# Kernel optimization log

Hardware: AMD Instinct MI355X
Metric: run time of the kernel (lower is better)

The kernel has to match this reference:

```python
import jax, jax.numpy as jnp
import numpy as np

IN_DIM = 768
D_MODEL = 256
B, T = 64, 2048
LN_EPS = 1e-5


def setup_inputs() -> dict:
    key = jax.random.key(0)
    ks = jax.random.split(key, 8)
    s_in = 1.0 / np.sqrt(IN_DIM)
    s_d = 1.0 / np.sqrt(D_MODEL)
    return {
        "x": jax.random.normal(ks[0], (B, T, IN_DIM), dtype=jnp.float32),
        "ln_gamma": jnp.ones((IN_DIM,), jnp.float32),
        "ln_beta": jnp.zeros((IN_DIM,), jnp.float32),
        "W_proj": jax.random.uniform(ks[1], (IN_DIM, D_MODEL), jnp.float32, -s_in, s_in),
        "b_proj": jax.random.uniform(ks[2], (D_MODEL,), jnp.float32, -s_in, s_in),
        "W1": jax.random.uniform(ks[3], (D_MODEL, D_MODEL), jnp.float32, -s_d, s_d),
        "b1": jax.random.uniform(ks[4], (D_MODEL,), jnp.float32, -s_d, s_d),
        "W2": jax.random.uniform(ks[5], (D_MODEL,), jnp.float32, -s_d, s_d),
        "b2": jax.random.uniform(ks[6], (), jnp.float32, -s_d, s_d),
    }


def reference(x, ln_gamma, ln_beta, W_proj, b_proj, W1, b1, W2, b2):
    # nan/inf sanitization to 0
    x = jnp.nan_to_num(x, nan=0.0, posinf=0.0, neginf=0.0)
    # LayerNorm over last dim (biased variance, eps=1e-5)
    mu = jnp.mean(x, axis=-1, keepdims=True)
    var = jnp.mean(jnp.square(x - mu), axis=-1, keepdims=True)
    xn = (x - mu) * jax.lax.rsqrt(var + LN_EPS) * ln_gamma + ln_beta
    # projection to d_model: [B, T, D]
    h = jnp.einsum('btf,fd->btd', xn, W_proj) + b_proj
    # tanh-MLP attention scores: [B, T]
    a = jnp.tanh(jnp.einsum('btd,de->bte', h, W1) + b1)
    w = jnp.einsum('bte,e->bt', a, W2) + b2
    w = jax.nn.softmax(w, axis=-1)
    # weighted-sum pooling over T: [B, D]
    return jnp.einsum('btd,bt->bd', h, w)
```

## Files before the change

### kernel.cpp

```cpp
#include <hip/hip_runtime.h>

#define LN_EPS 1e-5f

typedef __attribute__((ext_vector_type(8))) short s8vec;
typedef __attribute__((ext_vector_type(4))) float f4vec;

#define OFF_WPT   0u
#define OFF_W1T   393216u
#define OFF_U     524288u
#define OFF_C     525312u
#define OFF_UPART 526336u
#define OFF_VPART 575488u
#define OFF_PM    624640u
#define OFF_PS    632832u
#define OFF_PO    641024u

#define BAR()     asm volatile("s_barrier" ::: "memory")
#define WAIT_V4() asm volatile("s_waitcnt vmcnt(4) lgkmcnt(0)" ::: "memory")
#define WAIT_V0() asm volatile("s_waitcnt vmcnt(0) lgkmcnt(0)" ::: "memory")
#define WAIT_L0() asm volatile("s_waitcnt lgkmcnt(0)" ::: "memory")
#define ORDER_FENCE() do { asm volatile("" ::: "memory"); \
                           __builtin_amdgcn_sched_barrier(0); } while (0)

__device__ __forceinline__ unsigned short f2bf(float f) {
  unsigned int u = __float_as_uint(f);
  u += 0x7fffu + ((u >> 16) & 1u);
  return (unsigned short)(u >> 16);
}
__device__ __forceinline__ float bf2f(unsigned short h) {
  return __uint_as_float(((unsigned int)h) << 16);
}
__device__ __forceinline__ void gll16(const void* g, void* l) {
  __builtin_amdgcn_global_load_lds(
      (const __attribute__((address_space(1))) unsigned int*)g,
      (__attribute__((address_space(3))) unsigned int*)l, 16, 0, 0);
}

__global__ void k0_prep(const float* __restrict__ Wp,
                        const float* __restrict__ gamma,
                        const float* __restrict__ beta,
                        const float* __restrict__ W1,
                        char* __restrict__ ws) {
  const int blk = blockIdx.x;
  const int n = threadIdx.x;
  const int sw = (n & 7) << 4;
  if (blk < 48) {
    unsigned short* wpt = (unsigned short*)(ws + OFF_WPT);
    const int k0 = blk * 16;
    float up = 0.f, vp = 0.f;
#pragma unroll
    for (int j = 0; j < 16; ++j) {
      const int k = k0 + j;
      const float w = Wp[k * 256 + n];
      const float wpv = gamma[k] * w;
      up += wpv;
      vp += beta[k] * w;
      const int c = k >> 6, kc = k & 63;
      wpt[c * 16384 + n * 64 + ((((kc * 2) ^ sw)) >> 1)] = f2bf(wpv);
    }
    ((float*)(ws + OFF_UPART))[blk * 256 + n] = up;
    ((float*)(ws + OFF_VPART))[blk * 256 + n] = vp;
  } else {
    unsigned short* w1t = (unsigned short*)(ws + OFF_W1T);
    const int d0 = (blk - 48) * 16;
#pragma unroll
    for (int j = 0; j < 16; ++j) {
      const int d = d0 + j;
      const int c = d >> 6, dc = d & 63;
      w1t[c * 16384 + n * 64 + ((((dc * 2) ^ sw)) >> 1)] = f2bf(W1[d * 256 + n]);
    }
  }
}

__global__ void k0_reduce(const float* __restrict__ bproj, char* __restrict__ ws) {
  const int n = threadIdx.x;
  const float* upart = (const float*)(ws + OFF_UPART);
  const float* vpart = (const float*)(ws + OFF_VPART);
  float u = 0.f, v = 0.f;
  for (int i = 0; i < 48; ++i) {
    u += upart[i * 256 + n];
    v += vpart[i * 256 + n];
  }
  ((float*)(ws + OFF_U))[n] = u;
  ((float*)(ws + OFF_C))[n] = v + bproj[n];
}

__global__ __launch_bounds__(256, 2)
void k1_main(const float* __restrict__ x,
             const float* __restrict__ b1,
             const float* __restrict__ W2,
             char* __restrict__ ws) {
  __shared__ __align__(16) char sm_h[32768];
  __shared__ __align__(16) char sm_b[32768];
  __shared__ __align__(16) char sm_a[8192];
  __shared__ float sm_u[256], sm_c[256], sm_b1[256], sm_w2[256];
  __shared__ float sm_mu[64], sm_inv[64];
  __shared__ float sm_lp[64 * 4];
  __shared__ float sm_lg[64];
  __shared__ float sm_e[64];

  const int tid  = threadIdx.x;
  const int lane = tid & 63;
  const int wid  = tid >> 6;
  const int lr = lane & 15;
  const int lq = lane >> 4;

  sm_u[tid]  = ((const float*)(ws + OFF_U))[tid];
  sm_c[tid]  = ((const float*)(ws + OFF_C))[tid];
  sm_b1[tid] = b1[tid];
  sm_w2[tid] = W2[tid];

  const int arow = tid >> 2;
  const int aq   = tid & 3;
  const float* xrow = x + (size_t)(blockIdx.x * 64 + arow) * 768 + aq * 16;

  const char* bsrc  = (const char*)ws + OFF_WPT + wid * 8192 + lane * 16;
  const char* b2src = (const char*)ws + OFF_W1T + wid * 8192 + lane * 16;
  char*       bdst  = sm_b + wid * 8192 + lane * 16;

  const f4vec fz = {0.f, 0.f, 0.f, 0.f};
  f4vec acc[4][4];
#pragma unroll
  for (int m = 0; m < 4; ++m)
#pragma unroll
    for (int n = 0; n < 4; ++n) acc[m][n] = fz;

  float s1 = 0.f, s2 = 0.f;
  float4 vaA[4], vaB[4];
#pragma unroll
  for (int j = 0; j < 4; ++j) vaA[j] = *(const float4*)(xrow + 0 * 64 + j * 4);
#pragma unroll
  for (int j = 0; j < 4; ++j) vaB[j] = *(const float4*)(xrow + 1 * 64 + j * 4);

  auto p1body = [&](int c, float4 (&va)[4], bool pf) {
#pragma unroll
    for (int s = 0; s < 8; ++s) gll16(bsrc + c * 32768 + s * 1024, bdst + s * 1024);
    ORDER_FENCE();
    float v[16];
#pragma unroll
    for (int j = 0; j < 4; ++j) {
      v[4*j+0] = va[j].x; v[4*j+1] = va[j].y; v[4*j+2] = va[j].z; v[4*j+3] = va[j].w;
    }
    unsigned int pk[8];
#pragma unroll
    for (int j = 0; j < 16; ++j) {
      float f = v[j];
      if ((__float_as_uint(f) & 0x7f800000u) == 0x7f800000u) f = 0.f;
      s1 += f; s2 += f * f;
      const unsigned int hb = f2bf(f);
      if ((j & 1) == 0) pk[j >> 1] = hb; else pk[j >> 1] |= hb << 16;
    }
    {
      const int base = arow * 128 + aq * 32;
      const int sw = (arow & 7) << 4;
      *(int4*)(sm_a + ((base     ) ^ sw)) = make_int4((int)pk[0], (int)pk[1], (int)pk[2], (int)pk[3]);
      *(int4*)(sm_a + ((base + 16) ^ sw)) = make_int4((int)pk[4], (int)pk[5], (int)pk[6], (int)pk[7]);
    }
    if (pf) {
#pragma unroll
      for (int j = 0; j < 4; ++j) va[j] = *(const float4*)(xrow + (c + 2) * 64 + j * 4);
    }
    if (pf) WAIT_V4(); else WAIT_V0();
    BAR();
#pragma unroll
    for (int ks = 0; ks < 2; ++ks) {
      const int kb = (ks * 32 + lq * 8) * 2;
      s8vec af[4], bfv[4];
#pragma unroll
      for (int m = 0; m < 4; ++m) {
        const int row = m * 16 + lr;
        af[m] = *(const s8vec*)(sm_a + ((row * 128 + kb) ^ ((row & 7) << 4)));
      }
#pragma unroll
      for (int n = 0; n < 4; ++n) {
        const int row = wid * 64 + n * 16 + lr;
        bfv[n] = *(const s8vec*)(sm_b + ((row * 128 + kb) ^ ((row & 7) << 4)));
      }
#pragma unroll
      for (int m = 0; m < 4; ++m)
#pragma unroll
        for (int n = 0; n < 4; ++n)
          acc[m][n] = __builtin_amdgcn_mfma_f32_16x16x32_bf16(af[m], bfv[n], acc[m][n], 0, 0, 0);
    }
    BAR();
  };

  for (int cc = 0; cc < 12; cc += 2) {
    p1body(cc,     vaA, cc + 2 < 12);
    p1body(cc + 1, vaB, cc + 3 < 12);
  }

  s1 += __shfl_xor(s1, 1); s1 += __shfl_xor(s1, 2);
  s2 += __shfl_xor(s2, 1); s2 += __shfl_xor(s2, 2);
  if (aq == 0) {
    const float mu = s1 * (1.f / 768.f);
    float var = s2 * (1.f / 768.f) - mu * mu;
    var = fmaxf(var, 0.f);
    sm_mu[arow]  = mu;
    sm_inv[arow] = rsqrtf(var + LN_EPS);
  }
#pragma unroll
  for (int s = 0; s < 8; ++s) gll16(b2src + s * 1024, bdst + s * 1024);
  WAIT_L0();
  BAR();

#pragma unroll
  for (int m = 0; m < 4; ++m) {
#pragma unroll
    for (int i = 0; i < 4; ++i) {
      const int rl = m * 16 + lq * 4 + i;
      const float mu  = sm_mu[rl];
      const float inv = sm_inv[rl];
      const int sw = (rl & 7) << 4;
#pragma unroll
      for (int n = 0; n < 4; ++n) {
        const int cd = wid * 64 + n * 16 + lr;
        const float h = inv * (acc[m][n][i] - mu * sm_u[cd]) + sm_c[cd];
        *(unsigned short*)(sm_h + ((rl * 512 + cd * 2) ^ sw)) = f2bf(h);
      }
    }
  }
  WAIT_V0();
  BAR();

  f4vec acc2[4][4];
#pragma unroll
  for (int m = 0; m < 4; ++m)
#pragma unroll
    for (int n = 0; n < 4; ++n) acc2[m][n] = fz;

  for (int c = 0; c < 4; ++c) {
    s8vec af[2][4], bfv[2][4];
#pragma unroll
    for (int ks = 0; ks < 2; ++ks) {
      const int kh = (c * 64 + ks * 32 + lq * 8) * 2;
      const int kb = (ks * 32 + lq * 8) * 2;
#pragma unroll
      for (int m = 0; m < 4; ++m) {
        const int row = m * 16 + lr;
        af[ks][m] = *(const s8vec*)(sm_h + ((row * 512 + kh) ^ ((row & 7) << 4)));
      }
#pragma unroll
      for (int n = 0; n < 4; ++n) {
        const int row = wid * 64 + n * 16 + lr;
        bfv[ks][n] = *(const s8vec*)(sm_b + ((row * 128 + kb) ^ ((row & 7) << 4)));
      }
    }
    WAIT_L0();
    BAR();
    if (c < 3) {
#pragma unroll
      for (int s = 0; s < 8; ++s) gll16(b2src + (c + 1) * 32768 + s * 1024, bdst + s * 1024);
    }
#pragma unroll
    for (int ks = 0; ks < 2; ++ks)
#pragma unroll
      for (int m = 0; m < 4; ++m)
#pragma unroll
        for (int n = 0; n < 4; ++n)
          acc2[m][n] = __builtin_amdgcn_mfma_f32_16x16x32_bf16(af[ks][m], bfv[ks][n], acc2[m][n], 0, 0, 0);
    if (c < 3) WAIT_V0();
    BAR();
  }

  float lp[4][4];
#pragma unroll
  for (int m = 0; m < 4; ++m)
#pragma unroll
    for (int i = 0; i < 4; ++i) lp[m][i] = 0.f;

#pragma unroll
  for (int m = 0; m < 4; ++m) {
#pragma unroll
    for (int n = 0; n < 4; ++n) {
      const int cd = wid * 64 + n * 16 + lr;
      const float b1v = sm_b1[cd];
      const float w2v = sm_w2[cd];
#pragma unroll
      for (int i = 0; i < 4; ++i) {
        float z = acc2[m][n][i] + b1v;
        z = fminf(fmaxf(z, -15.f), 15.f);
        const float e2 = __expf(2.f * z);
        const float a = (e2 - 1.f) / (e2 + 1.f);
        lp[m][i] += a * w2v;
      }
    }
  }
#pragma unroll
  for (int m = 0; m < 4; ++m) {
#pragma unroll
    for (int i = 0; i < 4; ++i) {
      float t = lp[m][i];
      t += __shfl_xor(t, 1);
      t += __shfl_xor(t, 2);
      t += __shfl_xor(t, 4);
      t += __shfl_xor(t, 8);
      if (lr == 0) sm_lp[(m * 16 + lq * 4 + i) * 4 + wid] = t;
    }
  }
  __syncthreads();
  if (tid < 64)
    sm_lg[tid] = sm_lp[tid*4+0] + sm_lp[tid*4+1] + sm_lp[tid*4+2] + sm_lp[tid*4+3];
  __syncthreads();

  float mx = -1e30f;
  for (int r = 0; r < 64; ++r) mx = fmaxf(mx, sm_lg[r]);
  if (tid < 64) sm_e[tid] = __expf(sm_lg[tid] - mx);
  __syncthreads();

  {
    const int d = tid;
    float o = 0.f;
    for (int r = 0; r < 64; ++r) {
      const float ev = sm_e[r];
      const unsigned short hb =
          *(const unsigned short*)(sm_h + ((r * 512 + d * 2) ^ ((r & 7) << 4)));
      o += ev * bf2f(hb);
    }
    ((float*)(ws + OFF_PO))[blockIdx.x * 256 + d] = o;
  }
  if (tid == 0) {
    float s = 0.f;
    for (int r = 0; r < 64; ++r) s += sm_e[r];
    ((float*)(ws + OFF_PS))[blockIdx.x] = s;
    ((float*)(ws + OFF_PM))[blockIdx.x] = mx;
  }
}

__global__ void k2_combine(const char* __restrict__ ws, float* __restrict__ out) {
  const int b = blockIdx.x;
  const int d = threadIdx.x;
  const float* pm = (const float*)(ws + OFF_PM) + b * 32;
  const float* ps = (const float*)(ws + OFF_PS) + b * 32;
  const float* po = (const float*)(ws + OFF_PO) + (size_t)b * 32 * 256;
  float mx = -1e30f;
  for (int c = 0; c < 32; ++c) mx = fmaxf(mx, pm[c]);
  float num = 0.f, den = 0.f;
  for (int c = 0; c < 32; ++c) {
    const float al = __expf(pm[c] - mx);
    den += al * ps[c];
    num += al * po[c * 256 + d];
  }
  out[b * 256 + d] = num / den;
}

extern "C" void kernel_launch(void* const* d_in, const int* in_sizes, int n_in,
                              void* d_out, int out_size, void* d_ws, size_t ws_size,
                              hipStream_t stream) {
  const float* x     = (const float*)d_in[0];
  const float* gamma = (const float*)d_in[1];
  const float* beta  = (const float*)d_in[2];
  const float* Wp    = (const float*)d_in[3];
  const float* bproj = (const float*)d_in[4];
  const float* W1    = (const float*)d_in[5];
  const float* b1    = (const float*)d_in[6];
  const float* W2    = (const float*)d_in[7];
  char* ws = (char*)d_ws;
  float* out = (float*)d_out;

  k0_prep   <<<dim3(64),   dim3(256), 0, stream>>>(Wp, gamma, beta, W1, ws);
  k0_reduce <<<dim3(1),    dim3(256), 0, stream>>>(bproj, ws);
  k1_main   <<<dim3(2048), dim3(256), 0, stream>>>(x, b1, W2, ws);
  k2_combine<<<dim3(64),   dim3(256), 0, stream>>>(ws, out);
}
```

Baseline: 170.4 us.

## Double-buffer LDS for phase-1 GEMM with 32-wide K chunks and MFMA priority

The first GEMM (LayerNorm'd x times W_proj) now works in 32-column K chunks with ping-pong LDS buffers for both A and B. Staging the next chunk's weights and packing the next x chunk now overlap the MFMAs on the current buffer, and each step needs only one barrier instead of two. The prep kernel writes W_proj in a matching 32-column swizzled layout, and s_setprio raises wave priority around the MFMA blocks in both GEMMs. The cost is twice as many loop iterations with smaller per-step work, more barriers overall, and a narrower 4-way XOR swizzle that may bring back LDS bank conflicts.

```diff
diff --git a/kernel.cpp b/kernel.cpp
--- a/kernel.cpp
+++ b/kernel.cpp
@@ -16,7 +16,7 @@
 #define OFF_PO    641024u
 
 #define BAR()     asm volatile("s_barrier" ::: "memory")
-#define WAIT_V4() asm volatile("s_waitcnt vmcnt(4) lgkmcnt(0)" ::: "memory")
+#define WAIT_V2() asm volatile("s_waitcnt vmcnt(2) lgkmcnt(0)" ::: "memory")
 #define WAIT_V0() asm volatile("s_waitcnt vmcnt(0) lgkmcnt(0)" ::: "memory")
 #define WAIT_L0() asm volatile("s_waitcnt lgkmcnt(0)" ::: "memory")
 #define ORDER_FENCE() do { asm volatile("" ::: "memory"); \
@@ -43,9 +43,9 @@
                         char* __restrict__ ws) {
   const int blk = blockIdx.x;
   const int n = threadIdx.x;
-  const int sw = (n & 7) << 4;
   if (blk < 48) {
     unsigned short* wpt = (unsigned short*)(ws + OFF_WPT);
+    const int sw = (n & 3) << 4;
     const int k0 = blk * 16;
     float up = 0.f, vp = 0.f;
 #pragma unroll
@@ -55,13 +55,14 @@
       const float wpv = gamma[k] * w;
       up += wpv;
       vp += beta[k] * w;
-      const int c = k >> 6, kc = k & 63;
-      wpt[c * 16384 + n * 64 + ((((kc * 2) ^ sw)) >> 1)] = f2bf(wpv);
+      const int c = k >> 5, kc = k & 31;
+      wpt[c * 8192 + n * 32 + ((((kc * 2) ^ sw)) >> 1)] = f2bf(wpv);
     }
     ((float*)(ws + OFF_UPART))[blk * 256 + n] = up;
     ((float*)(ws + OFF_VPART))[blk * 256 + n] = vp;
   } else {
     unsigned short* w1t = (unsigned short*)(ws + OFF_W1T);
+    const int sw = (n & 7) << 4;
     const int d0 = (blk - 48) * 16;
 #pragma unroll
     for (int j = 0; j < 16; ++j) {
@@ -112,11 +113,10 @@
 
   const int arow = tid >> 2;
   const int aq   = tid & 3;
-  const float* xrow = x + (size_t)(blockIdx.x * 64 + arow) * 768 + aq * 16;
-
-  const char* bsrc  = (const char*)ws + OFF_WPT + wid * 8192 + lane * 16;
+  const float* xrow = x + (size_t)(blockIdx.x * 64 + arow) * 768 + aq * 8;
+
+  const char* bsrc  = (const char*)ws + OFF_WPT + wid * 4096 + lane * 16;
   const char* b2src = (const char*)ws + OFF_W1T + wid * 8192 + lane * 16;
-  char*       bdst  = sm_b + wid * 8192 + lane * 16;
 
   const f4vec fz = {0.f, 0.f, 0.f, 0.f};
   f4vec acc[4][4];
@@ -126,69 +126,84 @@
     for (int n = 0; n < 4; ++n) acc[m][n] = fz;
 
   float s1 = 0.f, s2 = 0.f;
-  float4 vaA[4], vaB[4];
-#pragma unroll
-  for (int j = 0; j < 4; ++j) vaA[j] = *(const float4*)(xrow + 0 * 64 + j * 4);
-#pragma unroll
-  for (int j = 0; j < 4; ++j) vaB[j] = *(const float4*)(xrow + 1 * 64 + j * 4);
-
-  auto p1body = [&](int c, float4 (&va)[4], bool pf) {
-#pragma unroll
-    for (int s = 0; s < 8; ++s) gll16(bsrc + c * 32768 + s * 1024, bdst + s * 1024);
-    ORDER_FENCE();
-    float v[16];
-#pragma unroll
-    for (int j = 0; j < 4; ++j) {
-      v[4*j+0] = va[j].x; v[4*j+1] = va[j].y; v[4*j+2] = va[j].z; v[4*j+3] = va[j].w;
-    }
-    unsigned int pk[8];
-#pragma unroll
-    for (int j = 0; j < 16; ++j) {
+  float4 xcE[2], xcO[2];
+  xcE[0] = *(const float4*)(xrow + 0);  xcE[1] = *(const float4*)(xrow + 4);
+  xcO[0] = *(const float4*)(xrow + 32); xcO[1] = *(const float4*)(xrow + 36);
+
+  auto stageB = [&](int t, int p) {
+#pragma unroll
+    for (int s = 0; s < 4; ++s)
+      gll16(bsrc + t * 16384 + s * 1024,
+            sm_b + p * 16384 + wid * 4096 + s * 1024 + lane * 16);
+  };
+  auto packA = [&](const float4 (&xc)[2], int p) {
+    float v[8];
+    v[0]=xc[0].x; v[1]=xc[0].y; v[2]=xc[0].z; v[3]=xc[0].w;
+    v[4]=xc[1].x; v[5]=xc[1].y; v[6]=xc[1].z; v[7]=xc[1].w;
+    unsigned int pk[4];
+#pragma unroll
+    for (int j = 0; j < 8; ++j) {
       float f = v[j];
       if ((__float_as_uint(f) & 0x7f800000u) == 0x7f800000u) f = 0.f;
       s1 += f; s2 += f * f;
       const unsigned int hb = f2bf(f);
       if ((j & 1) == 0) pk[j >> 1] = hb; else pk[j >> 1] |= hb << 16;
     }
-    {
-      const int base = arow * 128 + aq * 32;
-      const int sw = (arow & 7) << 4;
-      *(int4*)(sm_a + ((base     ) ^ sw)) = make_int4((int)pk[0], (int)pk[1], (int)pk[2], (int)pk[3]);
-      *(int4*)(sm_a + ((base + 16) ^ sw)) = make_int4((int)pk[4], (int)pk[5], (int)pk[6], (int)pk[7]);
-    }
-    if (pf) {
-#pragma unroll
-      for (int j = 0; j < 4; ++j) va[j] = *(const float4*)(xrow + (c + 2) * 64 + j * 4);
-    }
-    if (pf) WAIT_V4(); else WAIT_V0();
+    *(int4*)(sm_a + p * 4096 + ((arow * 64 + aq * 16) ^ ((arow & 3) << 4))) =
+        make_int4((int)pk[0], (int)pk[1], (int)pk[2], (int)pk[3]);
+  };
+  auto mfmaStep = [&](int p) {
+    s8vec af[4], bf[4];
+#pragma unroll
+    for (int m = 0; m < 4; ++m) {
+      const int row = m * 16 + lr;
+      af[m] = *(const s8vec*)(sm_a + p * 4096 +
+                              ((row * 64 + lq * 16) ^ ((row & 3) << 4)));
+    }
+#pragma unroll
+    for (int n = 0; n < 4; ++n) {
+      const int row = wid * 64 + n * 16 + lr;
+      bf[n] = *(const s8vec*)(sm_b + p * 16384 +
+                              ((row * 64 + lq * 16) ^ ((row & 3) << 4)));
+    }
+    __builtin_amdgcn_s_setprio(1);
+#pragma unroll
+    for (int m = 0; m < 4; ++m)
+#pragma unroll
+      for (int n = 0; n < 4; ++n)
+        acc[m][n] = __builtin_amdgcn_mfma_f32_16x16x32_bf16(af[m], bf[n], acc[m][n], 0, 0, 0);
+    __builtin_amdgcn_s_setprio(0);
+  };
+
+  stageB(0, 0); ORDER_FENCE();
+  packA(xcE, 0);
+  xcE[0] = *(const float4*)(xrow + 64); xcE[1] = *(const float4*)(xrow + 68);
+  WAIT_V2(); BAR();
+
+  for (int t = 0; t < 22; t += 2) {
+    stageB(t + 1, 1); ORDER_FENCE();
+    packA(xcO, 1);
+    xcO[0] = *(const float4*)(xrow + (t + 3) * 32);
+    xcO[1] = *(const float4*)(xrow + (t + 3) * 32 + 4);
+    mfmaStep(0);
+    WAIT_V2(); BAR();
+
+    stageB(t + 2, 0); ORDER_FENCE();
+    packA(xcE, 0);
+    if (t + 4 <= 23) {
+      xcE[0] = *(const float4*)(xrow + (t + 4) * 32);
+      xcE[1] = *(const float4*)(xrow + (t + 4) * 32 + 4);
+    }
+    mfmaStep(1);
+    if (t + 4 <= 23) WAIT_V2(); else WAIT_V0();
     BAR();
-#pragma unroll
-    for (int ks = 0; ks < 2; ++ks) {
-      const int kb = (ks * 32 + lq * 8) * 2;
-      s8vec af[4], bfv[4];
-#pragma unroll
-      for (int m = 0; m < 4; ++m) {
-        const int row = m * 16 + lr;
-        af[m] = *(const s8vec*)(sm_a + ((row * 128 + kb) ^ ((row & 7) << 4)));
-      }
-#pragma unroll
-      for (int n = 0; n < 4; ++n) {
-        const int row = wid * 64 + n * 16 + lr;
-        bfv[n] = *(const s8vec*)(sm_b + ((row * 128 + kb) ^ ((row & 7) << 4)));
-      }
-#pragma unroll
-      for (int m = 0; m < 4; ++m)
-#pragma unroll
-        for (int n = 0; n < 4; ++n)
-          acc[m][n] = __builtin_amdgcn_mfma_f32_16x16x32_bf16(af[m], bfv[n], acc[m][n], 0, 0, 0);
-    }
-    BAR();
-  };
-
-  for (int cc = 0; cc < 12; cc += 2) {
-    p1body(cc,     vaA, cc + 2 < 12);
-    p1body(cc + 1, vaB, cc + 3 < 12);
-  }
+  }
+  stageB(23, 1); ORDER_FENCE();
+  packA(xcO, 1);
+  mfmaStep(0);
+  WAIT_V0(); BAR();
+  mfmaStep(1);
+  BAR();
 
   s1 += __shfl_xor(s1, 1); s1 += __shfl_xor(s1, 2);
   s2 += __shfl_xor(s2, 1); s2 += __shfl_xor(s2, 2);
@@ -200,7 +215,8 @@
     sm_inv[arow] = rsqrtf(var + LN_EPS);
   }
 #pragma unroll
-  for (int s = 0; s < 8; ++s) gll16(b2src + s * 1024, bdst + s * 1024);
+  for (int s = 0; s < 8; ++s)
+    gll16(b2src + s * 1024, sm_b + wid * 8192 + s * 1024 + lane * 16);
   WAIT_L0();
   BAR();
 
@@ -250,8 +266,11 @@
     BAR();
     if (c < 3) {
 #pragma unroll
-      for (int s = 0; s < 8; ++s) gll16(b2src + (c + 1) * 32768 + s * 1024, bdst + s * 1024);
-    }
+      for (int s = 0; s < 8; ++s)
+        gll16(b2src + (c + 1) * 32768 + s * 1024,
+              sm_b + wid * 8192 + s * 1024 + lane * 16);
+    }
+    __builtin_amdgcn_s_setprio(1);
 #pragma unroll
     for (int ks = 0; ks < 2; ++ks)
 #pragma unroll
@@ -259,6 +278,7 @@
 #pragma unroll
         for (int n = 0; n < 4; ++n)
           acc2[m][n] = __builtin_amdgcn_mfma_f32_16x16x32_bf16(af[ks][m], bfv[ks][n], acc2[m][n], 0, 0, 0);
+    __builtin_amdgcn_s_setprio(0);
     if (c < 3) WAIT_V0();
     BAR();
   }
```

New measurement: 184.6 us. 1.08x slower.

## Alias LDS buffers and read W1 from global to fit three blocks per CU

Applied to the files above, without the earlier changes.

The separate h, B and a shared buffers are merged into one 40 KB union, with sm_h aliasing the weight staging area. This cuts LDS per block so launch bounds can be raised from 2 to 3 blocks per CU. The second GEMM no longer stages W1 chunks through LDS with barriers. Each wave now loads B fragments straight from a plain row-major W1 transpose in global memory, leaving the second GEMM exposed to global/L2 load latency. The higher occupancy target may also force register spills with the 16-element accumulator arrays.

```diff
diff --git a/kernel.cpp b/kernel.cpp
--- a/kernel.cpp
+++ b/kernel.cpp
@@ -43,9 +43,9 @@
                         char* __restrict__ ws) {
   const int blk = blockIdx.x;
   const int n = threadIdx.x;
-  const int sw = (n & 7) << 4;
   if (blk < 48) {
     unsigned short* wpt = (unsigned short*)(ws + OFF_WPT);
+    const int sw = (n & 7) << 4;
     const int k0 = blk * 16;
     float up = 0.f, vp = 0.f;
 #pragma unroll
@@ -66,8 +66,7 @@
 #pragma unroll
     for (int j = 0; j < 16; ++j) {
       const int d = d0 + j;
-      const int c = d >> 6, dc = d & 63;
-      w1t[c * 16384 + n * 64 + ((((dc * 2) ^ sw)) >> 1)] = f2bf(W1[d * 256 + n]);
+      w1t[n * 256 + d] = f2bf(W1[d * 256 + n]);
     }
   }
 }
@@ -85,20 +84,22 @@
   ((float*)(ws + OFF_C))[n] = v + bproj[n];
 }
 
-__global__ __launch_bounds__(256, 2)
+__global__ __launch_bounds__(256, 3)
 void k1_main(const float* __restrict__ x,
              const float* __restrict__ b1,
              const float* __restrict__ W2,
              char* __restrict__ ws) {
-  __shared__ __align__(16) char sm_h[32768];
-  __shared__ __align__(16) char sm_b[32768];
-  __shared__ __align__(16) char sm_a[8192];
+  __shared__ __align__(16) char sm_un[40960];
   __shared__ float sm_u[256], sm_c[256], sm_b1[256], sm_w2[256];
   __shared__ float sm_mu[64], sm_inv[64];
   __shared__ float sm_lp[64 * 4];
   __shared__ float sm_lg[64];
   __shared__ float sm_e[64];
 
+  char* const sm_a = sm_un;
+  char* const sm_b = sm_un + 8192;
+  char* const sm_h = sm_un + 8192;
+
   const int tid  = threadIdx.x;
   const int lane = tid & 63;
   const int wid  = tid >> 6;
@@ -114,9 +115,8 @@
   const int aq   = tid & 3;
   const float* xrow = x + (size_t)(blockIdx.x * 64 + arow) * 768 + aq * 16;
 
-  const char* bsrc  = (const char*)ws + OFF_WPT + wid * 8192 + lane * 16;
-  const char* b2src = (const char*)ws + OFF_W1T + wid * 8192 + lane * 16;
-  char*       bdst  = sm_b + wid * 8192 + lane * 16;
+  const char* bsrc = (const char*)ws + OFF_WPT + wid * 8192 + lane * 16;
+  char*       bdst = sm_b + wid * 8192 + lane * 16;
 
   const f4vec fz = {0.f, 0.f, 0.f, 0.f};
   f4vec acc[4][4];
@@ -199,8 +199,6 @@
     sm_mu[arow]  = mu;
     sm_inv[arow] = rsqrtf(var + LN_EPS);
   }
-#pragma unroll
-  for (int s = 0; s < 8; ++s) gll16(b2src + s * 1024, bdst + s * 1024);
   WAIT_L0();
   BAR();
 
@@ -220,47 +218,33 @@
       }
     }
   }
-  WAIT_V0();
+  WAIT_L0();
   BAR();
 
+  const unsigned short* w1t = (const unsigned short*)(ws + OFF_W1T);
   f4vec acc2[4][4];
 #pragma unroll
   for (int m = 0; m < 4; ++m)
 #pragma unroll
     for (int n = 0; n < 4; ++n) acc2[m][n] = fz;
 
-  for (int c = 0; c < 4; ++c) {
-    s8vec af[2][4], bfv[2][4];
-#pragma unroll
-    for (int ks = 0; ks < 2; ++ks) {
-      const int kh = (c * 64 + ks * 32 + lq * 8) * 2;
-      const int kb = (ks * 32 + lq * 8) * 2;
-#pragma unroll
-      for (int m = 0; m < 4; ++m) {
-        const int row = m * 16 + lr;
-        af[ks][m] = *(const s8vec*)(sm_h + ((row * 512 + kh) ^ ((row & 7) << 4)));
-      }
-#pragma unroll
-      for (int n = 0; n < 4; ++n) {
-        const int row = wid * 64 + n * 16 + lr;
-        bfv[ks][n] = *(const s8vec*)(sm_b + ((row * 128 + kb) ^ ((row & 7) << 4)));
-      }
-    }
-    WAIT_L0();
-    BAR();
-    if (c < 3) {
-#pragma unroll
-      for (int s = 0; s < 8; ++s) gll16(b2src + (c + 1) * 32768 + s * 1024, bdst + s * 1024);
-    }
-#pragma unroll
-    for (int ks = 0; ks < 2; ++ks)
-#pragma unroll
-      for (int m = 0; m < 4; ++m)
-#pragma unroll
-        for (int n = 0; n < 4; ++n)
-          acc2[m][n] = __builtin_amdgcn_mfma_f32_16x16x32_bf16(af[ks][m], bfv[ks][n], acc2[m][n], 0, 0, 0);
-    if (c < 3) WAIT_V0();
-    BAR();
+#pragma unroll
+  for (int ks = 0; ks < 8; ++ks) {
+    const int kh = (ks * 32 + lq * 8) * 2;
+    s8vec af[4], bfv[4];
+#pragma unroll
+    for (int m = 0; m < 4; ++m) {
+      const int row = m * 16 + lr;
+      af[m] = *(const s8vec*)(sm_h + ((row * 512 + kh) ^ ((row & 7) << 4)));
+    }
+#pragma unroll
+    for (int n = 0; n < 4; ++n)
+      bfv[n] = *(const s8vec*)(w1t + (wid * 64 + n * 16 + lr) * 256 + ks * 32 + lq * 8);
+#pragma unroll
+    for (int m = 0; m < 4; ++m)
+#pragma unroll
+      for (int n = 0; n < 4; ++n)
+        acc2[m][n] = __builtin_amdgcn_mfma_f32_16x16x32_bf16(af[m], bfv[n], acc2[m][n], 0, 0, 0);
   }
 
   float lp[4][4];
```

After: 211.2 us. 1.24x slower.
